# Kernel tuning notes

Hardware: AMD Instinct MI355X
Metric: run time of the kernel (lower is better)

The kernel has to match this reference:

```python
import math
import jax, jax.numpy as jnp
import numpy as np

SIN_DIM = 8
HEADS = 4
HID = 64
EMBED = 6 + 1 + 3 * SIN_DIM + 5 + 2  # 38


def _sinusoidal(v):
    # v: [N] -> [N, SIN_DIM], interleaved sin/cos as in torch.stack(...).flatten(-2)
    div = jnp.exp(jnp.arange(0, SIN_DIM, 2, dtype=jnp.float32) * (-math.log(10000.0) / SIN_DIM))
    scaled = v[:, None] * div  # [N, SIN_DIM//2]
    return jnp.stack([jnp.sin(scaled), jnp.cos(scaled)], axis=-1).reshape(v.shape[0], SIN_DIM)


def _feature_embed(x):
    nt = jnp.clip(x[:, 0].astype(jnp.int32), 0, 5)
    role = jnp.clip(x[:, 5].astype(jnp.int32), 0, 4)
    return jnp.concatenate([
        jax.nn.one_hot(nt, 6, dtype=x.dtype),
        jnp.log1p(x[:, 1])[:, None],
        _sinusoidal(x[:, 2]),
        _sinusoidal(x[:, 3]),
        _sinusoidal(x[:, 4] * 100.0),
        jax.nn.one_hot(role, 5, dtype=x.dtype),
        x[:, 6:7],
        x[:, 7:8],
    ], axis=-1)  # [N, 38]


def _gat(x, adj, W, a_src, a_dst, concat):
    N = x.shape[0]
    h = (x @ W).reshape(N, HEADS, HID)                       # [N,H,D]
    src = jnp.einsum('nhd,hd->nh', h, a_src)                 # [N,H]
    dst = jnp.einsum('nhd,hd->nh', h, a_dst)                 # [N,H]
    e = src[:, None, :] + dst[None, :, :]                    # [N,N,H]
    e = jnp.where(e > 0, e, 0.2 * e)                         # leaky_relu(0.2)
    e = jnp.where(adj[:, :, None] > 0, e, -jnp.inf)
    a = jax.nn.softmax(e, axis=1)                            # softmax over neighbors j
    out = jnp.einsum('njh,nhd->nhd'.replace('nj', 'ij').replace('nhd,', 'jhd,').replace('->nhd', '->ihd'), a, h) if False else jnp.einsum('ijh,jhd->ihd', a, h)
    if concat:
        return out.reshape(N, HEADS * HID)
    return out.mean(axis=1)


def _layernorm(x, g, b, eps=1e-5):
    mu = x.mean(axis=-1, keepdims=True)
    var = ((x - mu) ** 2).mean(axis=-1, keepdims=True)
    return (x - mu) / jnp.sqrt(var + eps) * g + b


def setup_inputs() -> dict:
    key = jax.random.key(0)
    ks = jax.random.split(key, 16)
    N, C = 4096, 512
    # raw node features per FeatureEmbedding docstring
    nt = jax.random.randint(ks[0], (N,), 0, 6).astype(jnp.float32)
    arity = jax.random.randint(ks[1], (N,), 0, 5).astype(jnp.float32)
    arg_pos = jax.random.randint(ks[2], (N,), 0, 8).astype(jnp.float32)
    depth = jax.random.randint(ks[3], (N,), 0, 12).astype(jnp.float32)
    age = jax.random.uniform(ks[4], (N,))
    role = jax.random.randint(ks[5], (N,), 0, 5).astype(jnp.float32)
    pol = jax.random.bernoulli(ks[6], 0.5, (N,)).astype(jnp.float32)
    eq = jax.random.bernoulli(ks[7], 0.2, (N,)).astype(jnp.float32)
    node_features = jnp.stack([nt, arity, arg_pos, depth, age, role, pol, eq], axis=-1)
    adj = (jax.random.uniform(ks[8], (N, N)) < 0.01).astype(jnp.float32)
    adj = jnp.maximum(adj, jnp.eye(N, dtype=jnp.float32))  # self-loops
    pm = (jax.random.uniform(ks[9], (C, N)) < (8.0 / N)).astype(jnp.float32)
    pool_matrix = pm / jnp.clip(pm.sum(axis=1, keepdims=True), 1.0, None)
    def xavier(k, shape):
        fan = shape[0] + shape[-1]
        return jax.random.normal(k, shape, dtype=jnp.float32) * math.sqrt(2.0 / fan)
    return {
        'node_features': node_features, 'adj': adj, 'pool_matrix': pool_matrix,
        'W1': xavier(ks[10], (EMBED, HID * HEADS)),
        'a_src1': xavier(ks[11], (HEADS, HID)), 'a_dst1': xavier(ks[12], (HEADS, HID)),
        'g1': jnp.ones((HID * HEADS,), jnp.float32), 'b1': jnp.zeros((HID * HEADS,), jnp.float32),
        'W2': xavier(ks[13], (HID * HEADS, HID * HEADS)),
        'a_src2': xavier(ks[14], (HEADS, HID)), 'a_dst2': xavier(ks[15], (HEADS, HID)),
        'g2': jnp.ones((HID,), jnp.float32), 'b2': jnp.zeros((HID,), jnp.float32),
        'Ws': xavier(jax.random.fold_in(key, 100), (HID, HID)), 'bs': jnp.zeros((HID,), jnp.float32),
        'Wo': xavier(jax.random.fold_in(key, 101), (HID, 1)), 'bo': jnp.zeros((1,), jnp.float32),
    }


def reference(node_features, adj, pool_matrix, W1, a_src1, a_dst1, g1, b1,
              W2, a_src2, a_dst2, g2, b2, Ws, bs, Wo, bo):
    x = _feature_embed(node_features)                         # [N, 38]
    # layer 1: concat heads -> [N, 256]
    x = jax.nn.elu(_layernorm(_gat(x, adj, W1, a_src1, a_dst1, True), g1, b1))
    # layer 2: mean over heads -> [N, 64]  (dropout is eval-mode no-op)
    x = jax.nn.elu(_layernorm(_gat(x, adj, W2, a_src2, a_dst2, False), g2, b2))
    clause_emb = pool_matrix @ x                               # [C, 64]
    h = jax.nn.relu(clause_emb @ Ws + bs)                      # MLP scorer
    return (h @ Wo + bo)[:, 0]                                 # [C]
```

## Files before the change

### kernel.cpp

```cpp
#include <hip/hip_runtime.h>
#include <math.h>

#define N 4096
#define C 512
#define EMB 38
#define HEADS 4
#define HID 64
#define F1 256
#define MAXN 128
#define R2 8

__device__ __forceinline__ float wr_sum(float v) {
#pragma unroll
    for (int o = 32; o > 0; o >>= 1) v += __shfl_xor(v, o);
    return v;
}
__device__ __forceinline__ float wr_max(float v) {
#pragma unroll
    for (int o = 32; o > 0; o >>= 1) v = fmaxf(v, __shfl_xor(v, o));
    return v;
}

__global__ __launch_bounds__(256) void k_build(const float* __restrict__ adj,
                                               int* __restrict__ cnt, int* __restrict__ idx) {
    int i = blockIdx.x;
    __shared__ int c;
    if (threadIdx.x == 0) c = 0;
    __syncthreads();
    const float4* row = (const float4*)(adj + (size_t)i * N);
    for (int v = threadIdx.x; v < N / 4; v += blockDim.x) {
        float4 a = row[v];
        if (a.x > 0.f) { int p = atomicAdd(&c, 1); if (p < MAXN) idx[i * MAXN + p] = 4 * v + 0; }
        if (a.y > 0.f) { int p = atomicAdd(&c, 1); if (p < MAXN) idx[i * MAXN + p] = 4 * v + 1; }
        if (a.z > 0.f) { int p = atomicAdd(&c, 1); if (p < MAXN) idx[i * MAXN + p] = 4 * v + 2; }
        if (a.w > 0.f) { int p = atomicAdd(&c, 1); if (p < MAXN) idx[i * MAXN + p] = 4 * v + 3; }
    }
    __syncthreads();
    if (threadIdx.x == 0) cnt[i] = min(c, MAXN);
}

__global__ __launch_bounds__(256) void k_gemm1(const float* __restrict__ nf, const float* __restrict__ W1,
                                               const float* __restrict__ asrc, const float* __restrict__ adst,
                                               float* __restrict__ h1, float* __restrict__ s1, float* __restrict__ d1) {
    int n0 = blockIdx.x * R2, tid = threadIdx.x;
    __shared__ float fs[R2][8];
    __shared__ float xs[R2][EMB + 2];
    if (tid < R2 * 8) fs[tid >> 3][tid & 7] = nf[(size_t)(n0 + (tid >> 3)) * 8 + (tid & 7)];
    __syncthreads();
    {
        int r = tid & 7;
        int t = tid >> 3;
        const float* f = fs[r];
        for (int pass = 0; pass < 2; ++pass, t += 32) {
            if (t >= EMB) break;
            float val;
            if (t < 6) { int nt = min(max((int)f[0], 0), 5); val = (t == nt) ? 1.f : 0.f; }
            else if (t == 6) val = log1pf(f[1]);
            else if (t < 31) {
                int q = (t - 7) & 7, s = (t - 7) >> 3, m = q >> 1;
                float base = (s == 0) ? f[2] : (s == 1) ? f[3] : f[4] * 100.f;
                float div = expf((2.f * m) * (-logf(10000.f) / 8.f));
                float sc = base * div;
                val = (q & 1) ? cosf(sc) : sinf(sc);
            }
            else if (t < 36) { int role = min(max((int)f[5], 0), 4); val = (t - 31 == role) ? 1.f : 0.f; }
            else val = (t == 36) ? f[6] : f[7];
            xs[r][t] = val;
        }
    }
    __syncthreads();
    float acc[R2];
#pragma unroll
    for (int r = 0; r < R2; ++r) acc[r] = 0.f;
#pragma unroll
    for (int k = 0; k < EMB; ++k) {
        float wv = W1[k * F1 + tid];
#pragma unroll
        for (int r = 0; r < R2; ++r) acc[r] = fmaf(xs[r][k], wv, acc[r]);
    }
    int h = tid >> 6, lane = tid & 63;
    float av = asrc[tid], dv = adst[tid];
#pragma unroll
    for (int r = 0; r < R2; ++r) {
        h1[(size_t)(n0 + r) * F1 + tid] = acc[r];
        float ss = wr_sum(acc[r] * av);
        float dd = wr_sum(acc[r] * dv);
        if (lane == 0) { s1[(n0 + r) * HEADS + h] = ss; d1[(n0 + r) * HEADS + h] = dd; }
    }
}

__global__ __launch_bounds__(256) void k_gemm2(const float* __restrict__ x1, const float* __restrict__ W2,
                                               const float* __restrict__ asrc, const float* __restrict__ adst,
                                               float* __restrict__ h2, float* __restrict__ s2, float* __restrict__ d2) {
    int n0 = blockIdx.x * R2, tid = threadIdx.x;
    __shared__ float4 xs4[R2][F1 / 4];
    {
        int r = tid >> 5, kk = tid & 31;
        const float4* x1v = (const float4*)x1;
        xs4[r][kk]      = x1v[(size_t)(n0 + r) * 64 + kk];
        xs4[r][kk + 32] = x1v[(size_t)(n0 + r) * 64 + kk + 32];
    }
    __syncthreads();
    float acc[R2];
#pragma unroll
    for (int r = 0; r < R2; ++r) acc[r] = 0.f;
    for (int kk = 0; kk < F1 / 4; ++kk) {
        float w0 = W2[(4 * kk + 0) * F1 + tid];
        float w1 = W2[(4 * kk + 1) * F1 + tid];
        float w2 = W2[(4 * kk + 2) * F1 + tid];
        float w3 = W2[(4 * kk + 3) * F1 + tid];
#pragma unroll
        for (int r = 0; r < R2; ++r) {
            float4 x = xs4[r][kk];
            acc[r] = fmaf(x.x, w0, fmaf(x.y, w1, fmaf(x.z, w2, fmaf(x.w, w3, acc[r]))));
        }
    }
    int h = tid >> 6, lane = tid & 63;
    float av = asrc[tid], dv = adst[tid];
#pragma unroll
    for (int r = 0; r < R2; ++r) {
        h2[(size_t)(n0 + r) * F1 + tid] = acc[r];
        float ss = wr_sum(acc[r] * av);
        float dd = wr_sum(acc[r] * dv);
        if (lane == 0) { s2[(n0 + r) * HEADS + h] = ss; d2[(n0 + r) * HEADS + h] = dd; }
    }
}

__global__ __launch_bounds__(256) void k_agg1(const float* __restrict__ h1, const float* __restrict__ s1,
                                              const float* __restrict__ d1, const int* __restrict__ cnt,
                                              const int* __restrict__ idx, const float* __restrict__ g,
                                              const float* __restrict__ b, float* __restrict__ xo) {
    int i = blockIdx.x, tid = threadIdx.x;
    int h = tid >> 6, lane = tid & 63;
    __shared__ int nbrs[MAXN];
    __shared__ float w[HEADS][MAXN];
    __shared__ float red[HEADS];
    int c = cnt[i];
    int c8 = (c + 7) & ~7;
    if (tid < c) nbrs[tid] = idx[i * MAXN + tid];
    if (tid >= c && tid < c8) {
        nbrs[tid] = i;
        w[0][tid] = 0.f; w[1][tid] = 0.f; w[2][tid] = 0.f; w[3][tid] = 0.f;
    }
    __syncthreads();
    float si = s1[i * HEADS + h];
    float m = -INFINITY;
    for (int jj = lane; jj < c; jj += 64) {
        float e = si + d1[nbrs[jj] * HEADS + h];
        e = e > 0.f ? e : 0.2f * e;
        w[h][jj] = e;
        m = fmaxf(m, e);
    }
    m = wr_max(m);
    float l = 0.f;
    for (int jj = lane; jj < c; jj += 64) {
        float t = expf(w[h][jj] - m);
        w[h][jj] = t;
        l += t;
    }
    l = wr_sum(l);
    float acc0 = 0.f, acc1 = 0.f;
    for (int jj = 0; jj < c8; jj += 8) {
        int n0 = nbrs[jj], n1 = nbrs[jj + 1], n2 = nbrs[jj + 2], n3 = nbrs[jj + 3];
        int n4 = nbrs[jj + 4], n5 = nbrs[jj + 5], n6 = nbrs[jj + 6], n7 = nbrs[jj + 7];
        float w0 = w[h][jj], w1 = w[h][jj + 1], w2 = w[h][jj + 2], w3 = w[h][jj + 3];
        float w4 = w[h][jj + 4], w5 = w[h][jj + 5], w6 = w[h][jj + 6], w7 = w[h][jj + 7];
        float v0 = h1[(size_t)n0 * F1 + tid], v1 = h1[(size_t)n1 * F1 + tid];
        float v2 = h1[(size_t)n2 * F1 + tid], v3 = h1[(size_t)n3 * F1 + tid];
        float v4 = h1[(size_t)n4 * F1 + tid], v5 = h1[(size_t)n5 * F1 + tid];
        float v6 = h1[(size_t)n6 * F1 + tid], v7 = h1[(size_t)n7 * F1 + tid];
        acc0 = fmaf(w0, v0, fmaf(w1, v1, fmaf(w2, v2, fmaf(w3, v3, acc0))));
        acc1 = fmaf(w4, v4, fmaf(w5, v5, fmaf(w6, v6, fmaf(w7, v7, acc1))));
    }
    float acc = (acc0 + acc1) / l;
    float s = wr_sum(acc);
    if (lane == 0) red[h] = s;
    __syncthreads();
    float mu = (red[0] + red[1] + red[2] + red[3]) * (1.f / F1);
    float dv = acc - mu;
    float s2 = wr_sum(dv * dv);
    __syncthreads();
    if (lane == 0) red[h] = s2;
    __syncthreads();
    float var = (red[0] + red[1] + red[2] + red[3]) * (1.f / F1);
    float y = dv * rsqrtf(var + 1e-5f) * g[tid] + b[tid];
    xo[(size_t)i * F1 + tid] = y > 0.f ? y : expm1f(y);
}

__global__ __launch_bounds__(256) void k_agg2(const float* __restrict__ h2, const float* __restrict__ s2,
                                              const float* __restrict__ d2, const int* __restrict__ cnt,
                                              const int* __restrict__ idx, const float* __restrict__ g,
                                              const float* __restrict__ b, float* __restrict__ xo) {
    int i = blockIdx.x, tid = threadIdx.x;
    int h = tid >> 6, lane = tid & 63;
    __shared__ int nbrs[MAXN];
    __shared__ float w[HEADS][MAXN];
    __shared__ float vals[F1];
    int c = cnt[i];
    int c8 = (c + 7) & ~7;
    if (tid < c) nbrs[tid] = idx[i * MAXN + tid];
    if (tid >= c && tid < c8) {
        nbrs[tid] = i;
        w[0][tid] = 0.f; w[1][tid] = 0.f; w[2][tid] = 0.f; w[3][tid] = 0.f;
    }
    __syncthreads();
    float si = s2[i * HEADS + h];
    float m = -INFINITY;
    for (int jj = lane; jj < c; jj += 64) {
        float e = si + d2[nbrs[jj] * HEADS + h];
        e = e > 0.f ? e : 0.2f * e;
        w[h][jj] = e;
        m = fmaxf(m, e);
    }
    m = wr_max(m);
    float l = 0.f;
    for (int jj = lane; jj < c; jj += 64) {
        float t = expf(w[h][jj] - m);
        w[h][jj] = t;
        l += t;
    }
    l = wr_sum(l);
    float acc0 = 0.f, acc1 = 0.f;
    for (int jj = 0; jj < c8; jj += 8) {
        int n0 = nbrs[jj], n1 = nbrs[jj + 1], n2 = nbrs[jj + 2], n3 = nbrs[jj + 3];
        int n4 = nbrs[jj + 4], n5 = nbrs[jj + 5], n6 = nbrs[jj + 6], n7 = nbrs[jj + 7];
        float w0 = w[h][jj], w1 = w[h][jj + 1], w2 = w[h][jj + 2], w3 = w[h][jj + 3];
        float w4 = w[h][jj + 4], w5 = w[h][jj + 5], w6 = w[h][jj + 6], w7 = w[h][jj + 7];
        float v0 = h2[(size_t)n0 * F1 + tid], v1 = h2[(size_t)n1 * F1 + tid];
        float v2 = h2[(size_t)n2 * F1 + tid], v3 = h2[(size_t)n3 * F1 + tid];
        float v4 = h2[(size_t)n4 * F1 + tid], v5 = h2[(size_t)n5 * F1 + tid];
        float v6 = h2[(size_t)n6 * F1 + tid], v7 = h2[(size_t)n7 * F1 + tid];
        acc0 = fmaf(w0, v0, fmaf(w1, v1, fmaf(w2, v2, fmaf(w3, v3, acc0))));
        acc1 = fmaf(w4, v4, fmaf(w5, v5, fmaf(w6, v6, fmaf(w7, v7, acc1))));
    }
    vals[tid] = (acc0 + acc1) / l;
    __syncthreads();
    if (tid < HID) {
        float mv = (vals[tid] + vals[tid + 64] + vals[tid + 128] + vals[tid + 192]) * 0.25f;
        float mu = wr_sum(mv) * (1.f / HID);
        float dv = mv - mu;
        float var = wr_sum(dv * dv) * (1.f / HID);
        float y = dv * rsqrtf(var + 1e-5f) * g[tid] + b[tid];
        xo[i * HID + tid] = y > 0.f ? y : expm1f(y);
    }
}

__global__ __launch_bounds__(256) void k_poolscore(const float* __restrict__ pm, const float* __restrict__ x2,
                                                   const float* __restrict__ Ws, const float* __restrict__ bs,
                                                   const float* __restrict__ Wo, const float* __restrict__ bo,
                                                   float* __restrict__ out) {
    int c = blockIdx.x, tid = threadIdx.x;
    int w = tid >> 6, lane = tid & 63;
    __shared__ float sacc[4][HID];
    __shared__ float ce_s[HID];
    float acc = 0.f;
    const float4* pmv = (const float4*)(pm + (size_t)c * N);
#pragma unroll
    for (int it = 0; it < 4; ++it) {
        int vi = w * 256 + it * 64 + lane;
        float4 p4 = pmv[vi];
        float pc[4] = {p4.x, p4.y, p4.z, p4.w};
#pragma unroll
        for (int comp = 0; comp < 4; ++comp) {
            unsigned long long msk = __ballot(pc[comp] != 0.f);
            while (msk) {
                int bpos = __ffsll(msk) - 1;
                msk &= msk - 1;
                float pj = __shfl(pc[comp], bpos);
                int j = (w * 256 + it * 64 + bpos) * 4 + comp;
                acc += pj * x2[(size_t)j * HID + lane];
            }
        }
    }
    sacc[w][lane] = acc;
    __syncthreads();
    if (w == 0) {
        ce_s[lane] = sacc[0][lane] + sacc[1][lane] + sacc[2][lane] + sacc[3][lane];
    }
    __syncthreads();
    if (w == 0) {
        float hd = bs[lane];
#pragma unroll 8
        for (int k = 0; k < HID; ++k) hd = fmaf(ce_s[k], Ws[k * HID + lane], hd);
        hd = fmaxf(hd, 0.f);
        float v = wr_sum(hd * Wo[lane]);
        if (lane == 0) out[c] = v + bo[0];
    }
}

extern "C" void kernel_launch(void* const* d_in, const int* in_sizes, int n_in,
                              void* d_out, int out_size, void* d_ws, size_t ws_size,
                              hipStream_t stream) {
    const float* nf  = (const float*)d_in[0];
    const float* adj = (const float*)d_in[1];
    const float* pm  = (const float*)d_in[2];
    const float* W1  = (const float*)d_in[3];
    const float* as1 = (const float*)d_in[4];
    const float* ad1 = (const float*)d_in[5];
    const float* g1  = (const float*)d_in[6];
    const float* b1  = (const float*)d_in[7];
    const float* W2  = (const float*)d_in[8];
    const float* as2 = (const float*)d_in[9];
    const float* ad2 = (const float*)d_in[10];
    const float* g2  = (const float*)d_in[11];
    const float* b2  = (const float*)d_in[12];
    const float* Ws  = (const float*)d_in[13];
    const float* bs  = (const float*)d_in[14];
    const float* Wo  = (const float*)d_in[15];
    const float* bo  = (const float*)d_in[16];
    float* out = (float*)d_out;

    float* p = (float*)d_ws;
    float* h1  = p; p += (size_t)N * F1;
    float* s1  = p; p += (size_t)N * HEADS;
    float* d1  = p; p += (size_t)N * HEADS;
    float* x1  = p; p += (size_t)N * F1;
    float* h2  = p; p += (size_t)N * F1;
    float* s2  = p; p += (size_t)N * HEADS;
    float* d2  = p; p += (size_t)N * HEADS;
    float* x2  = p; p += (size_t)N * HID;
    int* cnt = (int*)p;
    int* idx = cnt + N;

    k_build<<<N, 256, 0, stream>>>(adj, cnt, idx);
    k_gemm1<<<N / R2, 256, 0, stream>>>(nf, W1, as1, ad1, h1, s1, d1);
    k_agg1<<<N, 256, 0, stream>>>(h1, s1, d1, cnt, idx, g1, b1, x1);
    k_gemm2<<<N / R2, 256, 0, stream>>>(x1, W2, as2, ad2, h2, s2, d2);
    k_agg2<<<N, 256, 0, stream>>>(h2, s2, d2, cnt, idx, g2, b2, x2);
    k_poolscore<<<C, 256, 0, stream>>>(pm, x2, Ws, bs, Wo, bo, out);
}
```

Before: 202.6 us.

## Fuse adjacency build with GEMM1 and parallelize GAT aggregation across neighbors

Merges the adjacency-list build and the layer-1 projection into one launch, with the block index choosing the role. The layer-1 GEMM now reads four inputs at a time from a zero-padded shared row. Both aggregation kernels are restructured: edge scores for all heads are computed in one vectorized pass, and each wave takes a strided subset of neighbors and gathers full 256-wide rows with float4 loads, followed by a shared-memory reduction across waves. GEMM2 drops its shared-memory staging of x1 and reads inputs directly from global memory, which may add load latency.

```diff
diff --git a/kernel.cpp b/kernel.cpp
--- a/kernel.cpp
+++ b/kernel.cpp
@@ -9,6 +9,8 @@
 #define F1 256
 #define MAXN 128
 #define R2 8
+#define BUILD_BLKS (N)
+#define GEMM1_BLKS (N / R2)
 
 __device__ __forceinline__ float wr_sum(float v) {
 #pragma unroll
@@ -21,31 +23,34 @@
     return v;
 }
 
-__global__ __launch_bounds__(256) void k_build(const float* __restrict__ adj,
-                                               int* __restrict__ cnt, int* __restrict__ idx) {
-    int i = blockIdx.x;
-    __shared__ int c;
-    if (threadIdx.x == 0) c = 0;
-    __syncthreads();
-    const float4* row = (const float4*)(adj + (size_t)i * N);
-    for (int v = threadIdx.x; v < N / 4; v += blockDim.x) {
-        float4 a = row[v];
-        if (a.x > 0.f) { int p = atomicAdd(&c, 1); if (p < MAXN) idx[i * MAXN + p] = 4 * v + 0; }
-        if (a.y > 0.f) { int p = atomicAdd(&c, 1); if (p < MAXN) idx[i * MAXN + p] = 4 * v + 1; }
-        if (a.z > 0.f) { int p = atomicAdd(&c, 1); if (p < MAXN) idx[i * MAXN + p] = 4 * v + 2; }
-        if (a.w > 0.f) { int p = atomicAdd(&c, 1); if (p < MAXN) idx[i * MAXN + p] = 4 * v + 3; }
-    }
-    __syncthreads();
-    if (threadIdx.x == 0) cnt[i] = min(c, MAXN);
-}
-
-__global__ __launch_bounds__(256) void k_gemm1(const float* __restrict__ nf, const float* __restrict__ W1,
-                                               const float* __restrict__ asrc, const float* __restrict__ adst,
-                                               float* __restrict__ h1, float* __restrict__ s1, float* __restrict__ d1) {
-    int n0 = blockIdx.x * R2, tid = threadIdx.x;
+__global__ __launch_bounds__(256) void k_stage1(const float* __restrict__ adj,
+                                                int* __restrict__ cnt, int* __restrict__ idx,
+                                                const float* __restrict__ nf, const float* __restrict__ W1,
+                                                const float* __restrict__ asrc, const float* __restrict__ adst,
+                                                float* __restrict__ h1, float* __restrict__ s1, float* __restrict__ d1) {
+    int tid = threadIdx.x;
+    if (blockIdx.x < BUILD_BLKS) {
+        int i = blockIdx.x;
+        __shared__ int c;
+        if (tid == 0) c = 0;
+        __syncthreads();
+        const float4* row = (const float4*)(adj + (size_t)i * N);
+        for (int v = tid; v < N / 4; v += 256) {
+            float4 a = row[v];
+            if (a.x > 0.f) { int p = atomicAdd(&c, 1); if (p < MAXN) idx[i * MAXN + p] = 4 * v + 0; }
+            if (a.y > 0.f) { int p = atomicAdd(&c, 1); if (p < MAXN) idx[i * MAXN + p] = 4 * v + 1; }
+            if (a.z > 0.f) { int p = atomicAdd(&c, 1); if (p < MAXN) idx[i * MAXN + p] = 4 * v + 2; }
+            if (a.w > 0.f) { int p = atomicAdd(&c, 1); if (p < MAXN) idx[i * MAXN + p] = 4 * v + 3; }
+        }
+        __syncthreads();
+        if (tid == 0) cnt[i] = min(c, MAXN);
+        return;
+    }
+    int n0 = (blockIdx.x - BUILD_BLKS) * R2;
     __shared__ float fs[R2][8];
-    __shared__ float xs[R2][EMB + 2];
+    __shared__ float xs[R2][40];
     if (tid < R2 * 8) fs[tid >> 3][tid & 7] = nf[(size_t)(n0 + (tid >> 3)) * 8 + (tid & 7)];
+    if (tid < R2 * 2) xs[tid >> 1][38 + (tid & 1)] = 0.f;
     __syncthreads();
     {
         int r = tid & 7;
@@ -73,7 +78,19 @@
 #pragma unroll
     for (int r = 0; r < R2; ++r) acc[r] = 0.f;
 #pragma unroll
-    for (int k = 0; k < EMB; ++k) {
+    for (int kk = 0; kk < 9; ++kk) {
+        float w0 = W1[(4 * kk + 0) * F1 + tid];
+        float w1 = W1[(4 * kk + 1) * F1 + tid];
+        float w2 = W1[(4 * kk + 2) * F1 + tid];
+        float w3 = W1[(4 * kk + 3) * F1 + tid];
+#pragma unroll
+        for (int r = 0; r < R2; ++r) {
+            float4 x = *(const float4*)&xs[r][4 * kk];
+            acc[r] = fmaf(x.x, w0, fmaf(x.y, w1, fmaf(x.z, w2, fmaf(x.w, w3, acc[r]))));
+        }
+    }
+#pragma unroll
+    for (int k = 36; k < EMB; ++k) {
         float wv = W1[k * F1 + tid];
 #pragma unroll
         for (int r = 0; r < R2; ++r) acc[r] = fmaf(xs[r][k], wv, acc[r]);
@@ -93,27 +110,15 @@
                                                const float* __restrict__ asrc, const float* __restrict__ adst,
                                                float* __restrict__ h2, float* __restrict__ s2, float* __restrict__ d2) {
     int n0 = blockIdx.x * R2, tid = threadIdx.x;
-    __shared__ float4 xs4[R2][F1 / 4];
-    {
-        int r = tid >> 5, kk = tid & 31;
-        const float4* x1v = (const float4*)x1;
-        xs4[r][kk]      = x1v[(size_t)(n0 + r) * 64 + kk];
-        xs4[r][kk + 32] = x1v[(size_t)(n0 + r) * 64 + kk + 32];
-    }
-    __syncthreads();
     float acc[R2];
 #pragma unroll
     for (int r = 0; r < R2; ++r) acc[r] = 0.f;
-    for (int kk = 0; kk < F1 / 4; ++kk) {
-        float w0 = W2[(4 * kk + 0) * F1 + tid];
-        float w1 = W2[(4 * kk + 1) * F1 + tid];
-        float w2 = W2[(4 * kk + 2) * F1 + tid];
-        float w3 = W2[(4 * kk + 3) * F1 + tid];
-#pragma unroll
-        for (int r = 0; r < R2; ++r) {
-            float4 x = xs4[r][kk];
-            acc[r] = fmaf(x.x, w0, fmaf(x.y, w1, fmaf(x.z, w2, fmaf(x.w, w3, acc[r]))));
-        }
+#pragma unroll 4
+    for (int k = 0; k < F1; ++k) {
+        float wv = W2[k * F1 + tid];
+#pragma unroll
+        for (int r = 0; r < R2; ++r)
+            acc[r] = fmaf(x1[(size_t)(n0 + r) * F1 + k], wv, acc[r]);
     }
     int h = tid >> 6, lane = tid & 63;
     float av = asrc[tid], dv = adst[tid];
@@ -131,59 +136,71 @@
                                               const int* __restrict__ idx, const float* __restrict__ g,
                                               const float* __restrict__ b, float* __restrict__ xo) {
     int i = blockIdx.x, tid = threadIdx.x;
-    int h = tid >> 6, lane = tid & 63;
+    int wv = tid >> 6, lane = tid & 63;
     __shared__ int nbrs[MAXN];
-    __shared__ float w[HEADS][MAXN];
+    __shared__ float wts[HEADS][MAXN + 1];
+    __shared__ float lsum[HEADS];
+    __shared__ float sacc[4][F1];
     __shared__ float red[HEADS];
     int c = cnt[i];
-    int c8 = (c + 7) & ~7;
     if (tid < c) nbrs[tid] = idx[i * MAXN + tid];
-    if (tid >= c && tid < c8) {
-        nbrs[tid] = i;
-        w[0][tid] = 0.f; w[1][tid] = 0.f; w[2][tid] = 0.f; w[3][tid] = 0.f;
-    }
-    __syncthreads();
-    float si = s1[i * HEADS + h];
-    float m = -INFINITY;
-    for (int jj = lane; jj < c; jj += 64) {
-        float e = si + d1[nbrs[jj] * HEADS + h];
-        e = e > 0.f ? e : 0.2f * e;
-        w[h][jj] = e;
-        m = fmaxf(m, e);
-    }
-    m = wr_max(m);
-    float l = 0.f;
-    for (int jj = lane; jj < c; jj += 64) {
-        float t = expf(w[h][jj] - m);
-        w[h][jj] = t;
-        l += t;
-    }
-    l = wr_sum(l);
-    float acc0 = 0.f, acc1 = 0.f;
-    for (int jj = 0; jj < c8; jj += 8) {
-        int n0 = nbrs[jj], n1 = nbrs[jj + 1], n2 = nbrs[jj + 2], n3 = nbrs[jj + 3];
-        int n4 = nbrs[jj + 4], n5 = nbrs[jj + 5], n6 = nbrs[jj + 6], n7 = nbrs[jj + 7];
-        float w0 = w[h][jj], w1 = w[h][jj + 1], w2 = w[h][jj + 2], w3 = w[h][jj + 3];
-        float w4 = w[h][jj + 4], w5 = w[h][jj + 5], w6 = w[h][jj + 6], w7 = w[h][jj + 7];
-        float v0 = h1[(size_t)n0 * F1 + tid], v1 = h1[(size_t)n1 * F1 + tid];
-        float v2 = h1[(size_t)n2 * F1 + tid], v3 = h1[(size_t)n3 * F1 + tid];
-        float v4 = h1[(size_t)n4 * F1 + tid], v5 = h1[(size_t)n5 * F1 + tid];
-        float v6 = h1[(size_t)n6 * F1 + tid], v7 = h1[(size_t)n7 * F1 + tid];
-        acc0 = fmaf(w0, v0, fmaf(w1, v1, fmaf(w2, v2, fmaf(w3, v3, acc0))));
-        acc1 = fmaf(w4, v4, fmaf(w5, v5, fmaf(w6, v6, fmaf(w7, v7, acc1))));
-    }
-    float acc = (acc0 + acc1) / l;
-    float s = wr_sum(acc);
+    __syncthreads();
+    if (tid < c) {
+        float4 dd = ((const float4*)d1)[nbrs[tid]];
+        float4 ss = ((const float4*)s1)[i];
+        float e0 = ss.x + dd.x, e1 = ss.y + dd.y, e2 = ss.z + dd.z, e3 = ss.w + dd.w;
+        wts[0][tid] = e0 > 0.f ? e0 : 0.2f * e0;
+        wts[1][tid] = e1 > 0.f ? e1 : 0.2f * e1;
+        wts[2][tid] = e2 > 0.f ? e2 : 0.2f * e2;
+        wts[3][tid] = e3 > 0.f ? e3 : 0.2f * e3;
+    }
+    __syncthreads();
+    {
+        float m = -INFINITY;
+        for (int jj = lane; jj < c; jj += 64) m = fmaxf(m, wts[wv][jj]);
+        m = wr_max(m);
+        float l = 0.f;
+        for (int jj = lane; jj < c; jj += 64) { float t = expf(wts[wv][jj] - m); wts[wv][jj] = t; l += t; }
+        l = wr_sum(l);
+        if (lane == 0) lsum[wv] = l;
+    }
+    __syncthreads();
+    int hq = lane >> 4;
+    const float4* hv = (const float4*)h1;
+    float4 acc = {0.f, 0.f, 0.f, 0.f};
+    int jj = wv;
+    for (; jj + 4 < c; jj += 8) {
+        int na = nbrs[jj], nb = nbrs[jj + 4];
+        float wa = wts[hq][jj], wb = wts[hq][jj + 4];
+        float4 va = hv[(size_t)na * 64 + lane];
+        float4 vb = hv[(size_t)nb * 64 + lane];
+        acc.x = fmaf(wa, va.x, acc.x); acc.y = fmaf(wa, va.y, acc.y);
+        acc.z = fmaf(wa, va.z, acc.z); acc.w = fmaf(wa, va.w, acc.w);
+        acc.x = fmaf(wb, vb.x, acc.x); acc.y = fmaf(wb, vb.y, acc.y);
+        acc.z = fmaf(wb, vb.z, acc.z); acc.w = fmaf(wb, vb.w, acc.w);
+    }
+    for (; jj < c; jj += 4) {
+        int na = nbrs[jj];
+        float wa = wts[hq][jj];
+        float4 va = hv[(size_t)na * 64 + lane];
+        acc.x = fmaf(wa, va.x, acc.x); acc.y = fmaf(wa, va.y, acc.y);
+        acc.z = fmaf(wa, va.z, acc.z); acc.w = fmaf(wa, va.w, acc.w);
+    }
+    ((float4*)&sacc[wv][0])[lane] = acc;
+    __syncthreads();
+    int h = tid >> 6;
+    float tot = (sacc[0][tid] + sacc[1][tid] + sacc[2][tid] + sacc[3][tid]) / lsum[h];
+    float s = wr_sum(tot);
     if (lane == 0) red[h] = s;
     __syncthreads();
     float mu = (red[0] + red[1] + red[2] + red[3]) * (1.f / F1);
-    float dv = acc - mu;
-    float s2 = wr_sum(dv * dv);
+    float dvv = tot - mu;
+    float s2 = wr_sum(dvv * dvv);
     __syncthreads();
     if (lane == 0) red[h] = s2;
     __syncthreads();
     float var = (red[0] + red[1] + red[2] + red[3]) * (1.f / F1);
-    float y = dv * rsqrtf(var + 1e-5f) * g[tid] + b[tid];
+    float y = dvv * rsqrtf(var + 1e-5f) * g[tid] + b[tid];
     xo[(size_t)i * F1 + tid] = y > 0.f ? y : expm1f(y);
 }
 
@@ -192,56 +209,72 @@
                                               const int* __restrict__ idx, const float* __restrict__ g,
                                               const float* __restrict__ b, float* __restrict__ xo) {
     int i = blockIdx.x, tid = threadIdx.x;
-    int h = tid >> 6, lane = tid & 63;
+    int wv = tid >> 6, lane = tid & 63;
     __shared__ int nbrs[MAXN];
-    __shared__ float w[HEADS][MAXN];
-    __shared__ float vals[F1];
+    __shared__ float wts[HEADS][MAXN + 1];
+    __shared__ float lsum[HEADS];
+    __shared__ float sacc[4][F1];
     int c = cnt[i];
-    int c8 = (c + 7) & ~7;
     if (tid < c) nbrs[tid] = idx[i * MAXN + tid];
-    if (tid >= c && tid < c8) {
-        nbrs[tid] = i;
-        w[0][tid] = 0.f; w[1][tid] = 0.f; w[2][tid] = 0.f; w[3][tid] = 0.f;
-    }
-    __syncthreads();
-    float si = s2[i * HEADS + h];
-    float m = -INFINITY;
-    for (int jj = lane; jj < c; jj += 64) {
-        float e = si + d2[nbrs[jj] * HEADS + h];
-        e = e > 0.f ? e : 0.2f * e;
-        w[h][jj] = e;
-        m = fmaxf(m, e);
-    }
-    m = wr_max(m);
-    float l = 0.f;
-    for (int jj = lane; jj < c; jj += 64) {
-        float t = expf(w[h][jj] - m);
-        w[h][jj] = t;
-        l += t;
-    }
-    l = wr_sum(l);
-    float acc0 = 0.f, acc1 = 0.f;
-    for (int jj = 0; jj < c8; jj += 8) {
-        int n0 = nbrs[jj], n1 = nbrs[jj + 1], n2 = nbrs[jj + 2], n3 = nbrs[jj + 3];
-        int n4 = nbrs[jj + 4], n5 = nbrs[jj + 5], n6 = nbrs[jj + 6], n7 = nbrs[jj + 7];
-        float w0 = w[h][jj], w1 = w[h][jj + 1], w2 = w[h][jj + 2], w3 = w[h][jj + 3];
-        float w4 = w[h][jj + 4], w5 = w[h][jj + 5], w6 = w[h][jj + 6], w7 = w[h][jj + 7];
-        float v0 = h2[(size_t)n0 * F1 + tid], v1 = h2[(size_t)n1 * F1 + tid];
-        float v2 = h2[(size_t)n2 * F1 + tid], v3 = h2[(size_t)n3 * F1 + tid];
-        float v4 = h2[(size_t)n4 * F1 + tid], v5 = h2[(size_t)n5 * F1 + tid];
-        float v6 = h2[(size_t)n6 * F1 + tid], v7 = h2[(size_t)n7 * F1 + tid];
-        acc0 = fmaf(w0, v0, fmaf(w1, v1, fmaf(w2, v2, fmaf(w3, v3, acc0))));
-        acc1 = fmaf(w4, v4, fmaf(w5, v5, fmaf(w6, v6, fmaf(w7, v7, acc1))));
-    }
-    vals[tid] = (acc0 + acc1) / l;
-    __syncthreads();
-    if (tid < HID) {
-        float mv = (vals[tid] + vals[tid + 64] + vals[tid + 128] + vals[tid + 192]) * 0.25f;
+    __syncthreads();
+    if (tid < c) {
+        float4 dd = ((const float4*)d2)[nbrs[tid]];
+        float4 ss = ((const float4*)s2)[i];
+        float e0 = ss.x + dd.x, e1 = ss.y + dd.y, e2 = ss.z + dd.z, e3 = ss.w + dd.w;
+        wts[0][tid] = e0 > 0.f ? e0 : 0.2f * e0;
+        wts[1][tid] = e1 > 0.f ? e1 : 0.2f * e1;
+        wts[2][tid] = e2 > 0.f ? e2 : 0.2f * e2;
+        wts[3][tid] = e3 > 0.f ? e3 : 0.2f * e3;
+    }
+    __syncthreads();
+    {
+        float m = -INFINITY;
+        for (int jj = lane; jj < c; jj += 64) m = fmaxf(m, wts[wv][jj]);
+        m = wr_max(m);
+        float l = 0.f;
+        for (int jj = lane; jj < c; jj += 64) { float t = expf(wts[wv][jj] - m); wts[wv][jj] = t; l += t; }
+        l = wr_sum(l);
+        if (lane == 0) lsum[wv] = l;
+    }
+    __syncthreads();
+    int hq = lane >> 4;
+    const float4* hvv = (const float4*)h2;
+    float4 acc = {0.f, 0.f, 0.f, 0.f};
+    int jj = wv;
+    for (; jj + 4 < c; jj += 8) {
+        int na = nbrs[jj], nb = nbrs[jj + 4];
+        float wa = wts[hq][jj], wb = wts[hq][jj + 4];
+        float4 va = hvv[(size_t)na * 64 + lane];
+        float4 vb = hvv[(size_t)nb * 64 + lane];
+        acc.x = fmaf(wa, va.x, acc.x); acc.y = fmaf(wa, va.y, acc.y);
+        acc.z = fmaf(wa, va.z, acc.z); acc.w = fmaf(wa, va.w, acc.w);
+        acc.x = fmaf(wb, vb.x, acc.x); acc.y = fmaf(wb, vb.y, acc.y);
+        acc.z = fmaf(wb, vb.z, acc.z); acc.w = fmaf(wb, vb.w, acc.w);
+    }
+    for (; jj < c; jj += 4) {
+        int na = nbrs[jj];
+        float wa = wts[hq][jj];
+        float4 va = hvv[(size_t)na * 64 + lane];
+        acc.x = fmaf(wa, va.x, acc.x); acc.y = fmaf(wa, va.y, acc.y);
+        acc.z = fmaf(wa, va.z, acc.z); acc.w = fmaf(wa, va.w, acc.w);
+    }
+    ((float4*)&sacc[wv][0])[lane] = acc;
+    __syncthreads();
+    if (wv == 0) {
+        float t0 = 0.f, t1 = 0.f, t2 = 0.f, t3 = 0.f;
+#pragma unroll
+        for (int w = 0; w < 4; ++w) {
+            t0 += sacc[w][lane];
+            t1 += sacc[w][lane + 64];
+            t2 += sacc[w][lane + 128];
+            t3 += sacc[w][lane + 192];
+        }
+        float mv = (t0 / lsum[0] + t1 / lsum[1] + t2 / lsum[2] + t3 / lsum[3]) * 0.25f;
         float mu = wr_sum(mv) * (1.f / HID);
-        float dv = mv - mu;
-        float var = wr_sum(dv * dv) * (1.f / HID);
-        float y = dv * rsqrtf(var + 1e-5f) * g[tid] + b[tid];
-        xo[i * HID + tid] = y > 0.f ? y : expm1f(y);
+        float dvv = mv - mu;
+        float var = wr_sum(dvv * dvv) * (1.f / HID);
+        float y = dvv * rsqrtf(var + 1e-5f) * g[lane] + b[lane];
+        xo[i * HID + lane] = y > 0.f ? y : expm1f(y);
     }
 }
 
@@ -322,8 +355,7 @@
     int* cnt = (int*)p;
     int* idx = cnt + N;
 
-    k_build<<<N, 256, 0, stream>>>(adj, cnt, idx);
-    k_gemm1<<<N / R2, 256, 0, stream>>>(nf, W1, as1, ad1, h1, s1, d1);
+    k_stage1<<<BUILD_BLKS + GEMM1_BLKS, 256, 0, stream>>>(adj, cnt, idx, nf, W1, as1, ad1, h1, s1, d1);
     k_agg1<<<N, 256, 0, stream>>>(h1, s1, d1, cnt, idx, g1, b1, x1);
     k_gemm2<<<N / R2, 256, 0, stream>>>(x1, W2, as2, ad2, h2, s2, d2);
     k_agg2<<<N, 256, 0, stream>>>(h2, s2, d2, cnt, idx, g2, b2, x2);
```

Result: slower. 238.7 us (+17.8%).
